# Performance work log

Hardware: AMD Instinct MI355X
Metric: run time of the kernel (lower is better)

Reference implementation:

```python
import jax, jax.numpy as jnp
import numpy as np

B, P, ENC = 64, 49, 1280
T, V, E, H, A = 25, 10000, 512, 1024, 512


def setup_inputs() -> dict:
    key = jax.random.key(0)
    ks = jax.random.split(key, 20)
    s = 0.02
    return {
        "encoder_out": jax.random.normal(ks[0], (B, P, ENC), jnp.float32),
        "captions": jax.random.randint(ks[1], (B, T), 0, V, jnp.int32),
        "embed": jax.random.normal(ks[2], (V, E), jnp.float32) * s,
        "W_eatt": jax.random.normal(ks[3], (A, ENC), jnp.float32) * s,
        "b_eatt": jnp.zeros((A,), jnp.float32),
        "W_datt": jax.random.normal(ks[4], (A, H), jnp.float32) * s,
        "b_datt": jnp.zeros((A,), jnp.float32),
        "W_fatt": jax.random.normal(ks[5], (1, A), jnp.float32) * s,
        "b_fatt": jnp.zeros((1,), jnp.float32),
        "W_ih": jax.random.normal(ks[6], (4 * H, E + ENC), jnp.float32) * s,
        "b_ih": jnp.zeros((4 * H,), jnp.float32),
        "W_hh": jax.random.normal(ks[7], (4 * H, H), jnp.float32) * s,
        "b_hh": jnp.zeros((4 * H,), jnp.float32),
        "W_h0": jax.random.normal(ks[8], (H, ENC), jnp.float32) * s,
        "b_h0": jnp.zeros((H,), jnp.float32),
        "W_c0": jax.random.normal(ks[9], (H, ENC), jnp.float32) * s,
        "b_c0": jnp.zeros((H,), jnp.float32),
        "W_out": jax.random.normal(ks[10], (V, H), jnp.float32) * s,
        "b_out": jnp.zeros((V,), jnp.float32),
    }


def reference(encoder_out, captions, embed, W_eatt, b_eatt, W_datt, b_datt,
              W_fatt, b_fatt, W_ih, b_ih, W_hh, b_hh, W_h0, b_h0, W_c0, b_c0,
              W_out, b_out):
    emb = embed[captions]                       # [B,T,E]
    mean_enc = encoder_out.mean(axis=1)         # [B,ENC]
    h0 = mean_enc @ W_h0.T + b_h0               # [B,H]
    c0 = mean_enc @ W_c0.T + b_c0
    # encoder-side attention projection is step-invariant; hoist out of loop
    att1 = encoder_out @ W_eatt.T + b_eatt      # [B,P,A]
    nH = h0.shape[-1]

    def step(carry, x_t):
        h, c = carry
        att2 = h @ W_datt.T + b_datt                          # [B,A]
        e = (jax.nn.relu(att1 + att2[:, None, :]) @ W_fatt.T + b_fatt)[..., 0]  # [B,P]
        alpha = jax.nn.softmax(e, axis=1)
        ctx = jnp.einsum('bp,bpe->be', alpha, encoder_out)    # [B,ENC]
        gin = jnp.concatenate([x_t, ctx], axis=1)             # [B,E+ENC]
        gates = gin @ W_ih.T + b_ih + h @ W_hh.T + b_hh       # [B,4H]
        i, f, g, o = jnp.split(gates, 4, axis=1)
        c_new = jax.nn.sigmoid(f) * c + jax.nn.sigmoid(i) * jnp.tanh(g)
        h_new = jax.nn.sigmoid(o) * jnp.tanh(c_new)
        preds = h_new @ W_out.T + b_out                       # dropout in eval mode = identity
        return (h_new, c_new), preds

    xs = jnp.swapaxes(emb[:, :-1, :], 0, 1)     # [T-1,B,E]
    _, preds = jax.lax.scan(step, (h0, c0), xs)
    return jnp.swapaxes(preds, 0, 1)            # [B,T-1,V]
```

## Files before the change

### kernel.cpp

```cpp
#include <hip/hip_runtime.h>
#include <hip/hip_bf16.h>

typedef float  v4f __attribute__((ext_vector_type(4)));
typedef short  v8s __attribute__((ext_vector_type(8)));
typedef int    v4i __attribute__((ext_vector_type(4)));

#define DEV static __device__ __forceinline__

DEV float bf2f(unsigned short u) {
    union { unsigned int i; float f; } x; x.i = ((unsigned int)u) << 16; return x.f;
}
DEV unsigned short f2bf(float f) {
    union { float f; unsigned int i; } x; x.f = f;
    unsigned int r = x.i + 0x7fff + ((x.i >> 16) & 1);
    return (unsigned short)(r >> 16);
}
DEV float sigm(float x) { return 1.f / (1.f + __expf(-x)); }

DEV v4i pack8(const float* f) {
    v4i o;
#pragma unroll
    for (int q = 0; q < 4; ++q)
        ((unsigned int*)&o)[q] = (unsigned int)f2bf(f[2 * q]) |
                                 ((unsigned int)f2bf(f[2 * q + 1]) << 16);
    return o;
}
DEV float lo16(unsigned int x) { union { unsigned int i; float f; } u; u.i = x << 16; return u.f; }
DEV float hi16(unsigned int x) { union { unsigned int i; float f; } u; u.i = x & 0xffff0000u; return u.f; }

__global__ __launch_bounds__(256) void uber_init(
    const float* __restrict__ Wih, const float* __restrict__ Whh,
    const float* __restrict__ bih, const float* __restrict__ bhh,
    const float* __restrict__ WoutF, const float* __restrict__ WeattF,
    const float* __restrict__ WdattF, const float* __restrict__ Wh0F,
    const float* __restrict__ Wc0F, const float* __restrict__ enc,
    const int* __restrict__ caps, const float* __restrict__ embed,
    unsigned short* __restrict__ Wz, unsigned short* __restrict__ Woutb,
    unsigned short* __restrict__ Weattb, unsigned short* __restrict__ Wdattb,
    unsigned short* __restrict__ Wh0b, unsigned short* __restrict__ Wc0b,
    unsigned short* __restrict__ encb, unsigned short* __restrict__ embb,
    unsigned short* __restrict__ meanb, float* __restrict__ bz)
{
    const int i = (blockIdx.x * 256 + threadIdx.x) * 8;
    float f[8];
    if (i < 11534336) {
        int n = i / 2816, k = i - n * 2816;
        const float* src = (k < 1792) ? &Wih[n * 1792 + k] : &Whh[n * 1024 + (k - 1792)];
        *(v4f*)&f[0] = *(const v4f*)src; *(v4f*)&f[4] = *(const v4f*)(src + 4);
        *(v4i*)&Wz[i] = pack8(f);
    } else if (i < 21774336) {
        int j = i - 11534336;
        *(v4f*)&f[0] = *(const v4f*)&WoutF[j]; *(v4f*)&f[4] = *(const v4f*)&WoutF[j + 4];
        *(v4i*)&Woutb[j] = pack8(f);
    } else if (i < 22429696) {
        int j = i - 21774336;
        *(v4f*)&f[0] = *(const v4f*)&WeattF[j]; *(v4f*)&f[4] = *(const v4f*)&WeattF[j + 4];
        *(v4i*)&Weattb[j] = pack8(f);
    } else if (i < 22953984) {
        int j = i - 22429696;
        *(v4f*)&f[0] = *(const v4f*)&WdattF[j]; *(v4f*)&f[4] = *(const v4f*)&WdattF[j + 4];
        *(v4i*)&Wdattb[j] = pack8(f);
    } else if (i < 24264704) {
        int j = i - 22953984;
        *(v4f*)&f[0] = *(const v4f*)&Wh0F[j]; *(v4f*)&f[4] = *(const v4f*)&Wh0F[j + 4];
        *(v4i*)&Wh0b[j] = pack8(f);
    } else if (i < 25575424) {
        int j = i - 24264704;
        *(v4f*)&f[0] = *(const v4f*)&Wc0F[j]; *(v4f*)&f[4] = *(const v4f*)&Wc0F[j + 4];
        *(v4i*)&Wc0b[j] = pack8(f);
    } else if (i < 29589504) {
        int j = i - 25575424;
        *(v4f*)&f[0] = *(const v4f*)&enc[j]; *(v4f*)&f[4] = *(const v4f*)&enc[j + 4];
        *(v4i*)&encb[j] = pack8(f);
    } else if (i < 30375936) {
        int j = i - 29589504;
        int b = j / 12288, r = j - b * 12288, t = r / 512, e = r - t * 512;
        const float* src = &embed[caps[b * 25 + t] * 512 + e];
        *(v4f*)&f[0] = *(const v4f*)src; *(v4f*)&f[4] = *(const v4f*)(src + 4);
        *(v4i*)&embb[j] = pack8(f);
    } else if (i < 30457856) {
        int j = i - 30375936;
        int b = j / 1280, c = j - b * 1280;
#pragma unroll
        for (int q = 0; q < 8; ++q) f[q] = 0.f;
        for (int p = 0; p < 49; ++p) {
            const float* src = &enc[(b * 49 + p) * 1280 + c];
            v4f a = *(const v4f*)src, bq = *(const v4f*)(src + 4);
#pragma unroll
            for (int q = 0; q < 4; ++q) { f[q] += a[q]; f[q + 4] += bq[q]; }
        }
#pragma unroll
        for (int q = 0; q < 8; ++q) f[q] *= (1.f / 49.f);
        *(v4i*)&meanb[j] = pack8(f);
    } else if (i < 30461952) {
        int j = i - 30457856;
#pragma unroll
        for (int q = 0; q < 8; ++q) f[q] = bih[j + q] + bhh[j + q];
        *(v4f*)&bz[j] = *(v4f*)&f[0]; *(v4f*)&bz[j + 4] = *(v4f*)&f[4];
    }
}

template <int OUT_BF16>
__global__ __launch_bounds__(256) void gemm64_bn16(
    const unsigned short* __restrict__ Ag, int lda,
    const unsigned short* __restrict__ Bg, int K,
    const float* __restrict__ bias, void* __restrict__ Cg, int ldc)
{
    __shared__ unsigned short lA[64 * 264];
    __shared__ unsigned short lB[16 * 264];
    const int tid = threadIdx.x, lane = tid & 63, w = tid >> 6;
    const int nb = blockIdx.x * 16;
    const int rA = tid >> 5, cA = (tid & 31) * 8;
    v4f acc = {0.f, 0.f, 0.f, 0.f};
    v4i ra[8], rb[2];
#pragma unroll
    for (int i = 0; i < 8; ++i)
        ra[i] = *(const v4i*)&Ag[(rA + i * 8) * lda + cA];
#pragma unroll
    for (int i = 0; i < 2; ++i)
        rb[i] = *(const v4i*)&Bg[(nb + rA + i * 8) * K + cA];
    for (int kt = 0; kt < K; kt += 256) {
#pragma unroll
        for (int i = 0; i < 8; ++i) *(v4i*)&lA[(rA + i * 8) * 264 + cA] = ra[i];
#pragma unroll
        for (int i = 0; i < 2; ++i) *(v4i*)&lB[(rA + i * 8) * 264 + cA] = rb[i];
        __syncthreads();
        if (kt + 256 < K) {
#pragma unroll
            for (int i = 0; i < 8; ++i)
                ra[i] = *(const v4i*)&Ag[(rA + i * 8) * lda + kt + 256 + cA];
#pragma unroll
            for (int i = 0; i < 2; ++i)
                rb[i] = *(const v4i*)&Bg[(nb + rA + i * 8) * K + kt + 256 + cA];
        }
#pragma unroll
        for (int ks = 0; ks < 8; ++ks) {
            v8s a = *(const v8s*)&lA[(w * 16 + (lane & 15)) * 264 + ks * 32 + (lane >> 4) * 8];
            v8s b = *(const v8s*)&lB[(lane & 15) * 264 + ks * 32 + (lane >> 4) * 8];
            acc = __builtin_amdgcn_mfma_f32_16x16x32_bf16(a, b, acc, 0, 0, 0);
        }
        __syncthreads();
    }
    const int n = nb + (lane & 15);
    const float bs = bias[n];
#pragma unroll
    for (int r = 0; r < 4; ++r) {
        int m = w * 16 + (lane >> 4) * 4 + r;
        float v = acc[r] + bs;
        if (OUT_BF16) ((unsigned short*)Cg)[m * ldc + n] = f2bf(v);
        else          ((float*)Cg)[m * ldc + n] = v;
    }
}

__global__ __launch_bounds__(256) void gemm_att1_k(
    const unsigned short* __restrict__ Aenc, const unsigned short* __restrict__ Bw,
    const float* __restrict__ bias, unsigned short* __restrict__ Cout)
{
    __shared__ unsigned short lA[64 * 136];
    __shared__ unsigned short lB[64 * 136];
    const int tid = threadIdx.x, lane = tid & 63, w = tid >> 6;
    const int mb = blockIdx.y * 64, nb = blockIdx.x * 64;
    const int rT = tid >> 4, cT = (tid & 15) * 8;
    v4f acc[4];
#pragma unroll
    for (int f = 0; f < 4; ++f) acc[f] = (v4f){0.f, 0.f, 0.f, 0.f};
    v4i ra[4], rb[4];
#pragma unroll
    for (int i = 0; i < 4; ++i) {
        ra[i] = *(const v4i*)&Aenc[(mb + rT + i * 16) * 1280 + cT];
        rb[i] = *(const v4i*)&Bw[(nb + rT + i * 16) * 1280 + cT];
    }
    for (int kt = 0; kt < 1280; kt += 128) {
#pragma unroll
        for (int i = 0; i < 4; ++i) {
            *(v4i*)&lA[(rT + i * 16) * 136 + cT] = ra[i];
            *(v4i*)&lB[(rT + i * 16) * 136 + cT] = rb[i];
        }
        __syncthreads();
        if (kt + 128 < 1280) {
#pragma unroll
            for (int i = 0; i < 4; ++i) {
                ra[i] = *(const v4i*)&Aenc[(mb + rT + i * 16) * 1280 + kt + 128 + cT];
                rb[i] = *(const v4i*)&Bw[(nb + rT + i * 16) * 1280 + kt + 128 + cT];
            }
        }
#pragma unroll
        for (int ks = 0; ks < 4; ++ks) {
            v8s a = *(const v8s*)&lA[(w * 16 + (lane & 15)) * 136 + ks * 32 + (lane >> 4) * 8];
#pragma unroll
            for (int f = 0; f < 4; ++f) {
                v8s b = *(const v8s*)&lB[(f * 16 + (lane & 15)) * 136 + ks * 32 + (lane >> 4) * 8];
                acc[f] = __builtin_amdgcn_mfma_f32_16x16x32_bf16(a, b, acc[f], 0, 0, 0);
            }
        }
        __syncthreads();
    }
#pragma unroll
    for (int f = 0; f < 4; ++f) {
        int n = nb + f * 16 + (lane & 15);
        float bs = bias[n];
#pragma unroll
        for (int r = 0; r < 4; ++r) {
            int m = mb + w * 16 + (lane >> 4) * 4 + r;
            Cout[m * 512 + n] = f2bf(acc[f][r] + bs);
        }
    }
}

__global__ __launch_bounds__(256) void attn_ctx_k(
    const float* __restrict__ att2, const unsigned short* __restrict__ att1b,
    const float* __restrict__ Wfatt, const float* __restrict__ bfatt,
    const unsigned short* __restrict__ encb, const unsigned short* __restrict__ embb,
    unsigned short* __restrict__ z, int tstep)
{
    __shared__ float a2[512];
    __shared__ float wf[512];
    __shared__ float es[64];
    __shared__ float alpha[64];
    const int tid = threadIdx.x, lane = tid & 63, w = tid >> 6;
    const int b = blockIdx.x;
    a2[tid]       = att2[b * 512 + tid];
    a2[tid + 256] = att2[b * 512 + tid + 256];
    wf[tid]       = Wfatt[tid];
    wf[tid + 256] = Wfatt[tid + 256];
    __syncthreads();
    for (int p = w; p < 49; p += 4) {
        v4i u = *(const v4i*)&att1b[(b * 49 + p) * 512 + lane * 8];
        v4f c0 = *(const v4f*)&a2[lane * 8], c1 = *(const v4f*)&a2[lane * 8 + 4];
        v4f w0 = *(const v4f*)&wf[lane * 8], w1 = *(const v4f*)&wf[lane * 8 + 4];
        float s = 0.f;
#pragma unroll
        for (int q = 0; q < 4; ++q) {
            unsigned int x = ((unsigned int*)&u)[q];
            float vlo = lo16(x), vhi = hi16(x);
            float clo = (q < 2) ? c0[q * 2] : c1[q * 2 - 4];
            float chi = (q < 2) ? c0[q * 2 + 1] : c1[q * 2 - 3];
            float wlo = (q < 2) ? w0[q * 2] : w1[q * 2 - 4];
            float whi = (q < 2) ? w0[q * 2 + 1] : w1[q * 2 - 3];
            s += fmaxf(vlo + clo, 0.f) * wlo;
            s += fmaxf(vhi + chi, 0.f) * whi;
        }
#pragma unroll
        for (int off = 32; off > 0; off >>= 1) s += __shfl_xor(s, off);
        if (lane == 0) es[p] = s + bfatt[0];
    }
    __syncthreads();
    if (w == 0) {
        float v = (lane < 49) ? es[lane] : -1e30f;
        float m = v;
#pragma unroll
        for (int off = 32; off > 0; off >>= 1) m = fmaxf(m, __shfl_xor(m, off));
        float e = (lane < 49) ? __expf(v - m) : 0.f;
        float s = e;
#pragma unroll
        for (int off = 32; off > 0; off >>= 1) s += __shfl_xor(s, off);
        if (lane < 49) alpha[lane] = e / s;
    }
    __syncthreads();
    if (tid < 160) {
        const int jb = tid * 8;
        float acc[8];
#pragma unroll
        for (int q = 0; q < 8; ++q) acc[q] = 0.f;
        for (int p = 0; p < 49; ++p) {
            v4i u = *(const v4i*)&encb[(b * 49 + p) * 1280 + jb];
            float al = alpha[p];
#pragma unroll
            for (int q = 0; q < 4; ++q) {
                unsigned int x = ((unsigned int*)&u)[q];
                acc[2 * q]     += al * lo16(x);
                acc[2 * q + 1] += al * hi16(x);
            }
        }
        *(v4i*)&z[b * 2816 + 512 + jb] = pack8(acc);
    }
    if (tid < 64)
        *(v4i*)&z[b * 2816 + tid * 8] = *(const v4i*)&embb[(b * 24 + tstep) * 512 + tid * 8];
}

__global__ __launch_bounds__(256) void gates_lstm_k(
    const unsigned short* __restrict__ z, const unsigned short* __restrict__ Wz,
    const float* __restrict__ bz, float* __restrict__ cst,
    unsigned short* __restrict__ zh, unsigned short* __restrict__ HallT)
{
    __shared__ unsigned short lA[64 * 264];
    __shared__ unsigned short lB[16 * 264];
    __shared__ float gbuf[64 * 20];
    const int tid = threadIdx.x, lane = tid & 63, w = tid >> 6;
    const int hb = blockIdx.x * 4;
    const int rT = tid >> 5, cT = (tid & 31) * 8;
    const int gate = rT & 3, hco = rT >> 2;
    const int growB = (gate * 1024 + hb + hco) * 2816;
    const int growB2 = (((rT + 8) & 3) * 1024 + hb + ((rT + 8) >> 2)) * 2816;
    v4f acc = {0.f, 0.f, 0.f, 0.f};
    v4i ra[8], rb[2];
#pragma unroll
    for (int i = 0; i < 8; ++i)
        ra[i] = *(const v4i*)&z[(rT + i * 8) * 2816 + cT];
    rb[0] = *(const v4i*)&Wz[growB + cT];
    rb[1] = *(const v4i*)&Wz[growB2 + cT];
    for (int kt = 0; kt < 2816; kt += 256) {
#pragma unroll
        for (int i = 0; i < 8; ++i) *(v4i*)&lA[(rT + i * 8) * 264 + cT] = ra[i];
        *(v4i*)&lB[rT * 264 + cT] = rb[0];
        *(v4i*)&lB[(rT + 8) * 264 + cT] = rb[1];
        __syncthreads();
        if (kt + 256 < 2816) {
#pragma unroll
            for (int i = 0; i < 8; ++i)
                ra[i] = *(const v4i*)&z[(rT + i * 8) * 2816 + kt + 256 + cT];
            rb[0] = *(const v4i*)&Wz[growB + kt + 256 + cT];
            rb[1] = *(const v4i*)&Wz[growB2 + kt + 256 + cT];
        }
#pragma unroll
        for (int ks = 0; ks < 8; ++ks) {
            v8s a = *(const v8s*)&lA[(w * 16 + (lane & 15)) * 264 + ks * 32 + (lane >> 4) * 8];
            v8s b = *(const v8s*)&lB[(lane & 15) * 264 + ks * 32 + (lane >> 4) * 8];
            acc = __builtin_amdgcn_mfma_f32_16x16x32_bf16(a, b, acc, 0, 0, 0);
        }
        __syncthreads();
    }
#pragma unroll
    for (int r = 0; r < 4; ++r) {
        int m = w * 16 + (lane >> 4) * 4 + r;
        int n = lane & 15;
        gbuf[m * 20 + n] = acc[r];
    }
    __syncthreads();
    const int b = tid >> 2, hc2 = tid & 3, hidx = hb + hc2;
    float gi = gbuf[b * 20 + hc2 * 4 + 0] + bz[hidx];
    float gf = gbuf[b * 20 + hc2 * 4 + 1] + bz[1024 + hidx];
    float gg = gbuf[b * 20 + hc2 * 4 + 2] + bz[2048 + hidx];
    float go = gbuf[b * 20 + hc2 * 4 + 3] + bz[3072 + hidx];
    float cn = sigm(gf) * cst[b * 1024 + hidx] + sigm(gi) * tanhf(gg);
    float hn = sigm(go) * tanhf(cn);
    cst[b * 1024 + hidx] = cn;
    unsigned short hb16 = f2bf(hn);
    zh[b * 2816 + hidx] = hb16;
    HallT[b * 1024 + hidx] = hb16;
}

__global__ __launch_bounds__(256) void preds_k(
    const unsigned short* __restrict__ Hall, const unsigned short* __restrict__ Wout,
    const float* __restrict__ bout, float* __restrict__ out)
{
    __shared__ unsigned short lA[128 * 72];
    __shared__ unsigned short lB[128 * 72];
    const int tid = threadIdx.x, lane = tid & 63, w = tid >> 6;
    const int mb = blockIdx.y * 128, nb = blockIdx.x * 128;
    const int rT = tid >> 3, cT = (tid & 7) * 8;
    int nB = nb + rT; if (nB > 9999) nB = 9999;
    v4f acc[2][8];
#pragma unroll
    for (int i = 0; i < 2; ++i)
#pragma unroll
        for (int f = 0; f < 8; ++f) acc[i][f] = (v4f){0.f, 0.f, 0.f, 0.f};
    v4i ra[4], rb[4];
#pragma unroll
    for (int i = 0; i < 4; ++i) {
        ra[i] = *(const v4i*)&Hall[(mb + rT + i * 32) * 1024 + cT];
        int n2 = nb + rT + i * 32; if (n2 > 9999) n2 = 9999;
        rb[i] = *(const v4i*)&Wout[n2 * 1024 + cT];
    }
    for (int kt = 0; kt < 1024; kt += 64) {
#pragma unroll
        for (int i = 0; i < 4; ++i) {
            *(v4i*)&lA[(rT + i * 32) * 72 + cT] = ra[i];
            *(v4i*)&lB[(rT + i * 32) * 72 + cT] = rb[i];
        }
        __syncthreads();
        if (kt + 64 < 1024) {
#pragma unroll
            for (int i = 0; i < 4; ++i) {
                ra[i] = *(const v4i*)&Hall[(mb + rT + i * 32) * 1024 + kt + 64 + cT];
                int n2 = nb + rT + i * 32; if (n2 > 9999) n2 = 9999;
                rb[i] = *(const v4i*)&Wout[n2 * 1024 + kt + 64 + cT];
            }
        }
#pragma unroll
        for (int ks = 0; ks < 2; ++ks) {
            int ko = ks * 32 + (lane >> 4) * 8;
            v8s a0 = *(const v8s*)&lA[(w * 32 + (lane & 15)) * 72 + ko];
            v8s a1 = *(const v8s*)&lA[(w * 32 + 16 + (lane & 15)) * 72 + ko];
#pragma unroll
            for (int f = 0; f < 8; ++f) {
                v8s b = *(const v8s*)&lB[(f * 16 + (lane & 15)) * 72 + ko];
                acc[0][f] = __builtin_amdgcn_mfma_f32_16x16x32_bf16(a0, b, acc[0][f], 0, 0, 0);
                acc[1][f] = __builtin_amdgcn_mfma_f32_16x16x32_bf16(a1, b, acc[1][f], 0, 0, 0);
            }
        }
        __syncthreads();
    }
#pragma unroll
    for (int f = 0; f < 8; ++f) {
        int n = nb + f * 16 + (lane & 15);
        if (n < 10000) {
            float bs = bout[n];
#pragma unroll
            for (int i = 0; i < 2; ++i)
#pragma unroll
                for (int r = 0; r < 4; ++r) {
                    int m = mb + w * 32 + i * 16 + (lane >> 4) * 4 + r;
                    int tt = m >> 6, bb = m & 63;
                    out[(bb * 24 + tt) * 10000 + n] = acc[i][f][r] + bs;
                }
        }
    }
}

extern "C" void kernel_launch(void* const* d_in, const int* in_sizes, int n_in,
                              void* d_out, int out_size, void* d_ws, size_t ws_size,
                              hipStream_t stream)
{
    const float* enc   = (const float*)d_in[0];
    const int*   caps  = (const int*)d_in[1];
    const float* embed = (const float*)d_in[2];
    const float* Weatt = (const float*)d_in[3];
    const float* beatt = (const float*)d_in[4];
    const float* Wdatt = (const float*)d_in[5];
    const float* bdatt = (const float*)d_in[6];
    const float* Wfatt = (const float*)d_in[7];
    const float* bfatt = (const float*)d_in[8];
    const float* Wih   = (const float*)d_in[9];
    const float* bih   = (const float*)d_in[10];
    const float* Whh   = (const float*)d_in[11];
    const float* bhh   = (const float*)d_in[12];
    const float* Wh0   = (const float*)d_in[13];
    const float* bh0   = (const float*)d_in[14];
    const float* Wc0   = (const float*)d_in[15];
    const float* bc0   = (const float*)d_in[16];
    const float* WoutF = (const float*)d_in[17];
    const float* bout  = (const float*)d_in[18];
    float* out = (float*)d_out;

    char* ws = (char*)d_ws;
    size_t off = 0;
    auto carve = [&](size_t bytes) -> void* {
        void* p = ws + off; off += (bytes + 255) & ~(size_t)255; return p;
    };
    unsigned short* Wzb    = (unsigned short*)carve(11534336ull * 2);
    unsigned short* Woutb  = (unsigned short*)carve(10240000ull * 2);
    unsigned short* Weattb = (unsigned short*)carve(655360ull * 2);
    unsigned short* Wdattb = (unsigned short*)carve(524288ull * 2);
    unsigned short* Wh0b   = (unsigned short*)carve(1310720ull * 2);
    unsigned short* Wc0b   = (unsigned short*)carve(1310720ull * 2);
    unsigned short* encb   = (unsigned short*)carve(4014080ull * 2);
    unsigned short* embb   = (unsigned short*)carve(786432ull * 2);
    unsigned short* meanb  = (unsigned short*)carve(81920ull * 2);
    unsigned short* att1b  = (unsigned short*)carve(1605632ull * 2);
    unsigned short* Hallb  = (unsigned short*)carve(1572864ull * 2);
    unsigned short* zb     = (unsigned short*)carve(180224ull * 2);
    float* bz   = (float*)carve(4096ull * 4);
    float* att2 = (float*)carve(32768ull * 4);
    float* cst  = (float*)carve(65536ull * 4);

    uber_init<<<14874, 256, 0, stream>>>(Wih, Whh, bih, bhh, WoutF, Weatt, Wdatt,
        Wh0, Wc0, enc, caps, embed, Wzb, Woutb, Weattb, Wdattb, Wh0b, Wc0b,
        encb, embb, meanb, bz);

    gemm64_bn16<1><<<64, 256, 0, stream>>>(meanb, 1280, Wh0b, 1280, bh0, zb + 1792, 2816);
    gemm64_bn16<0><<<64, 256, 0, stream>>>(meanb, 1280, Wc0b, 1280, bc0, cst, 1024);

    gemm_att1_k<<<dim3(8, 49), 256, 0, stream>>>(encb, Weattb, beatt, att1b);

    for (int t = 0; t < 24; ++t) {
        gemm64_bn16<0><<<32, 256, 0, stream>>>(zb + 1792, 2816, Wdattb, 1024, bdatt, att2, 512);
        attn_ctx_k<<<64, 256, 0, stream>>>(att2, att1b, Wfatt, bfatt, encb, embb, zb, t);
        gates_lstm_k<<<256, 256, 0, stream>>>(zb, Wzb, bz, cst, zb + 1792,
                                              Hallb + (size_t)t * 64 * 1024);
    }

    preds_k<<<dim3(79, 12), 256, 0, stream>>>(Hallb, Woutb, bout, out);
}
```

Baseline: 1.137 ms.

## Replace per-step LSTM kernel launches with a persistent grid-barrier kernel

```diff
diff --git a/kernel.cpp b/kernel.cpp
--- a/kernel.cpp
+++ b/kernel.cpp
@@ -28,58 +28,62 @@
 DEV float lo16(unsigned int x) { union { unsigned int i; float f; } u; u.i = x << 16; return u.f; }
 DEV float hi16(unsigned int x) { union { unsigned int i; float f; } u; u.i = x & 0xffff0000u; return u.f; }
 
+__global__ void bar_init_k(int* __restrict__ bars) {
+    bars[blockIdx.x * 256 + threadIdx.x] = 0;
+}
+
+DEV void gridbar(int* bars, int idx) {
+    __syncthreads();
+    if (threadIdx.x == 0) {
+        __builtin_amdgcn_fence(__ATOMIC_RELEASE, "");
+        int* base = bars + idx * 160;
+        const int grp = blockIdx.x & 7;
+        int old = __hip_atomic_fetch_add(base + grp * 16, 1, __ATOMIC_RELAXED,
+                                         __HIP_MEMORY_SCOPE_SYSTEM);
+        if (old == 31) {
+            int og = __hip_atomic_fetch_add(base + 128, 1, __ATOMIC_RELAXED,
+                                            __HIP_MEMORY_SCOPE_SYSTEM);
+            if (og == 7)
+                __hip_atomic_store(base + 144, 1, __ATOMIC_RELAXED,
+                                   __HIP_MEMORY_SCOPE_SYSTEM);
+        }
+        while (!__hip_atomic_load(base + 144, __ATOMIC_RELAXED,
+                                  __HIP_MEMORY_SCOPE_SYSTEM))
+            __builtin_amdgcn_s_sleep(2);
+        __builtin_amdgcn_fence(__ATOMIC_ACQUIRE, "");
+    }
+    __syncthreads();
+}
+
 __global__ __launch_bounds__(256) void uber_init(
-    const float* __restrict__ Wih, const float* __restrict__ Whh,
-    const float* __restrict__ bih, const float* __restrict__ bhh,
     const float* __restrict__ WoutF, const float* __restrict__ WeattF,
-    const float* __restrict__ WdattF, const float* __restrict__ Wh0F,
-    const float* __restrict__ Wc0F, const float* __restrict__ enc,
-    const int* __restrict__ caps, const float* __restrict__ embed,
-    unsigned short* __restrict__ Wz, unsigned short* __restrict__ Woutb,
-    unsigned short* __restrict__ Weattb, unsigned short* __restrict__ Wdattb,
-    unsigned short* __restrict__ Wh0b, unsigned short* __restrict__ Wc0b,
+    const float* __restrict__ enc, const int* __restrict__ caps,
+    const float* __restrict__ embed,
+    unsigned short* __restrict__ Woutb, unsigned short* __restrict__ Weattb,
     unsigned short* __restrict__ encb, unsigned short* __restrict__ embb,
-    unsigned short* __restrict__ meanb, float* __restrict__ bz)
+    float* __restrict__ meanf)
 {
     const int i = (blockIdx.x * 256 + threadIdx.x) * 8;
     float f[8];
-    if (i < 11534336) {
-        int n = i / 2816, k = i - n * 2816;
-        const float* src = (k < 1792) ? &Wih[n * 1792 + k] : &Whh[n * 1024 + (k - 1792)];
-        *(v4f*)&f[0] = *(const v4f*)src; *(v4f*)&f[4] = *(const v4f*)(src + 4);
-        *(v4i*)&Wz[i] = pack8(f);
-    } else if (i < 21774336) {
-        int j = i - 11534336;
-        *(v4f*)&f[0] = *(const v4f*)&WoutF[j]; *(v4f*)&f[4] = *(const v4f*)&WoutF[j + 4];
-        *(v4i*)&Woutb[j] = pack8(f);
-    } else if (i < 22429696) {
-        int j = i - 21774336;
+    if (i < 10240000) {
+        *(v4f*)&f[0] = *(const v4f*)&WoutF[i]; *(v4f*)&f[4] = *(const v4f*)&WoutF[i + 4];
+        *(v4i*)&Woutb[i] = pack8(f);
+    } else if (i < 10895360) {
+        int j = i - 10240000;
         *(v4f*)&f[0] = *(const v4f*)&WeattF[j]; *(v4f*)&f[4] = *(const v4f*)&WeattF[j + 4];
         *(v4i*)&Weattb[j] = pack8(f);
-    } else if (i < 22953984) {
-        int j = i - 22429696;
-        *(v4f*)&f[0] = *(const v4f*)&WdattF[j]; *(v4f*)&f[4] = *(const v4f*)&WdattF[j + 4];
-        *(v4i*)&Wdattb[j] = pack8(f);
-    } else if (i < 24264704) {
-        int j = i - 22953984;
-        *(v4f*)&f[0] = *(const v4f*)&Wh0F[j]; *(v4f*)&f[4] = *(const v4f*)&Wh0F[j + 4];
-        *(v4i*)&Wh0b[j] = pack8(f);
-    } else if (i < 25575424) {
-        int j = i - 24264704;
-        *(v4f*)&f[0] = *(const v4f*)&Wc0F[j]; *(v4f*)&f[4] = *(const v4f*)&Wc0F[j + 4];
-        *(v4i*)&Wc0b[j] = pack8(f);
-    } else if (i < 29589504) {
-        int j = i - 25575424;
+    } else if (i < 14909440) {
+        int j = i - 10895360;
         *(v4f*)&f[0] = *(const v4f*)&enc[j]; *(v4f*)&f[4] = *(const v4f*)&enc[j + 4];
         *(v4i*)&encb[j] = pack8(f);
-    } else if (i < 30375936) {
-        int j = i - 29589504;
+    } else if (i < 15695872) {
+        int j = i - 14909440;
         int b = j / 12288, r = j - b * 12288, t = r / 512, e = r - t * 512;
         const float* src = &embed[caps[b * 25 + t] * 512 + e];
         *(v4f*)&f[0] = *(const v4f*)src; *(v4f*)&f[4] = *(const v4f*)(src + 4);
         *(v4i*)&embb[j] = pack8(f);
-    } else if (i < 30457856) {
-        int j = i - 30375936;
+    } else if (i < 15777792) {
+        int j = i - 15695872;
         int b = j / 1280, c = j - b * 1280;
 #pragma unroll
         for (int q = 0; q < 8; ++q) f[q] = 0.f;
@@ -91,64 +95,8 @@
         }
 #pragma unroll
         for (int q = 0; q < 8; ++q) f[q] *= (1.f / 49.f);
-        *(v4i*)&meanb[j] = pack8(f);
-    } else if (i < 30461952) {
-        int j = i - 30457856;
-#pragma unroll
-        for (int q = 0; q < 8; ++q) f[q] = bih[j + q] + bhh[j + q];
-        *(v4f*)&bz[j] = *(v4f*)&f[0]; *(v4f*)&bz[j + 4] = *(v4f*)&f[4];
-    }
-}
-
-template <int OUT_BF16>
-__global__ __launch_bounds__(256) void gemm64_bn16(
-    const unsigned short* __restrict__ Ag, int lda,
-    const unsigned short* __restrict__ Bg, int K,
-    const float* __restrict__ bias, void* __restrict__ Cg, int ldc)
-{
-    __shared__ unsigned short lA[64 * 264];
-    __shared__ unsigned short lB[16 * 264];
-    const int tid = threadIdx.x, lane = tid & 63, w = tid >> 6;
-    const int nb = blockIdx.x * 16;
-    const int rA = tid >> 5, cA = (tid & 31) * 8;
-    v4f acc = {0.f, 0.f, 0.f, 0.f};
-    v4i ra[8], rb[2];
-#pragma unroll
-    for (int i = 0; i < 8; ++i)
-        ra[i] = *(const v4i*)&Ag[(rA + i * 8) * lda + cA];
-#pragma unroll
-    for (int i = 0; i < 2; ++i)
-        rb[i] = *(const v4i*)&Bg[(nb + rA + i * 8) * K + cA];
-    for (int kt = 0; kt < K; kt += 256) {
-#pragma unroll
-        for (int i = 0; i < 8; ++i) *(v4i*)&lA[(rA + i * 8) * 264 + cA] = ra[i];
-#pragma unroll
-        for (int i = 0; i < 2; ++i) *(v4i*)&lB[(rA + i * 8) * 264 + cA] = rb[i];
-        __syncthreads();
-        if (kt + 256 < K) {
-#pragma unroll
-            for (int i = 0; i < 8; ++i)
-                ra[i] = *(const v4i*)&Ag[(rA + i * 8) * lda + kt + 256 + cA];
-#pragma unroll
-            for (int i = 0; i < 2; ++i)
-                rb[i] = *(const v4i*)&Bg[(nb + rA + i * 8) * K + kt + 256 + cA];
-        }
-#pragma unroll
-        for (int ks = 0; ks < 8; ++ks) {
-            v8s a = *(const v8s*)&lA[(w * 16 + (lane & 15)) * 264 + ks * 32 + (lane >> 4) * 8];
-            v8s b = *(const v8s*)&lB[(lane & 15) * 264 + ks * 32 + (lane >> 4) * 8];
-            acc = __builtin_amdgcn_mfma_f32_16x16x32_bf16(a, b, acc, 0, 0, 0);
-        }
-        __syncthreads();
-    }
-    const int n = nb + (lane & 15);
-    const float bs = bias[n];
-#pragma unroll
-    for (int r = 0; r < 4; ++r) {
-        int m = w * 16 + (lane >> 4) * 4 + r;
-        float v = acc[r] + bs;
-        if (OUT_BF16) ((unsigned short*)Cg)[m * ldc + n] = f2bf(v);
-        else          ((float*)Cg)[m * ldc + n] = v;
+        *(v4f*)&meanf[j] = *(v4f*)&f[0];
+        *(v4f*)&meanf[j + 4] = *(v4f*)&f[4];
     }
 }
 
@@ -207,149 +155,211 @@
     }
 }
 
-__global__ __launch_bounds__(256) void attn_ctx_k(
-    const float* __restrict__ att2, const unsigned short* __restrict__ att1b,
+__global__ __launch_bounds__(256, 1) void pers_k(
+    const float* __restrict__ Wih, const float* __restrict__ Whh,
+    const float* __restrict__ bih, const float* __restrict__ bhh,
+    const float* __restrict__ Wdatt, const float* __restrict__ bdatt,
     const float* __restrict__ Wfatt, const float* __restrict__ bfatt,
-    const unsigned short* __restrict__ encb, const unsigned short* __restrict__ embb,
-    unsigned short* __restrict__ z, int tstep)
+    const float* __restrict__ Wh0, const float* __restrict__ bh0,
+    const float* __restrict__ Wc0, const float* __restrict__ bc0,
+    const float* __restrict__ meanf,
+    const unsigned short* __restrict__ att1b,
+    const unsigned short* __restrict__ encb,
+    const unsigned short* __restrict__ embb,
+    unsigned short* __restrict__ z, float* __restrict__ att2,
+    unsigned short* __restrict__ Hall, int* __restrict__ bars)
 {
-    __shared__ float a2[512];
+    __shared__ unsigned short lWz[16 * 2824];
+    __shared__ unsigned short lWd[16 * 1032];
+    __shared__ float gbuf[64 * 20];
+    __shared__ float a2f[512];
     __shared__ float wf[512];
     __shared__ float es[64];
     __shared__ float alpha[64];
+    __shared__ float bzs[16];
+
     const int tid = threadIdx.x, lane = tid & 63, w = tid >> 6;
-    const int b = blockIdx.x;
-    a2[tid]       = att2[b * 512 + tid];
-    a2[tid + 256] = att2[b * 512 + tid + 256];
-    wf[tid]       = Wfatt[tid];
-    wf[tid + 256] = Wfatt[tid + 256];
-    __syncthreads();
-    for (int p = w; p < 49; p += 4) {
-        v4i u = *(const v4i*)&att1b[(b * 49 + p) * 512 + lane * 8];
-        v4f c0 = *(const v4f*)&a2[lane * 8], c1 = *(const v4f*)&a2[lane * 8 + 4];
-        v4f w0 = *(const v4f*)&wf[lane * 8], w1 = *(const v4f*)&wf[lane * 8 + 4];
-        float s = 0.f;
-#pragma unroll
-        for (int q = 0; q < 4; ++q) {
-            unsigned int x = ((unsigned int*)&u)[q];
-            float vlo = lo16(x), vhi = hi16(x);
-            float clo = (q < 2) ? c0[q * 2] : c1[q * 2 - 4];
-            float chi = (q < 2) ? c0[q * 2 + 1] : c1[q * 2 - 3];
-            float wlo = (q < 2) ? w0[q * 2] : w1[q * 2 - 4];
-            float whi = (q < 2) ? w0[q * 2 + 1] : w1[q * 2 - 3];
-            s += fmaxf(vlo + clo, 0.f) * wlo;
-            s += fmaxf(vhi + chi, 0.f) * whi;
-        }
-#pragma unroll
-        for (int off = 32; off > 0; off >>= 1) s += __shfl_xor(s, off);
-        if (lane == 0) es[p] = s + bfatt[0];
-    }
-    __syncthreads();
-    if (w == 0) {
-        float v = (lane < 49) ? es[lane] : -1e30f;
-        float m = v;
-#pragma unroll
-        for (int off = 32; off > 0; off >>= 1) m = fmaxf(m, __shfl_xor(m, off));
-        float e = (lane < 49) ? __expf(v - m) : 0.f;
-        float s = e;
-#pragma unroll
-        for (int off = 32; off > 0; off >>= 1) s += __shfl_xor(s, off);
-        if (lane < 49) alpha[lane] = e / s;
-    }
-    __syncthreads();
-    if (tid < 160) {
-        const int jb = tid * 8;
-        float acc[8];
-#pragma unroll
-        for (int q = 0; q < 8; ++q) acc[q] = 0.f;
-        for (int p = 0; p < 49; ++p) {
-            v4i u = *(const v4i*)&encb[(b * 49 + p) * 1280 + jb];
-            float al = alpha[p];
-#pragma unroll
-            for (int q = 0; q < 4; ++q) {
-                unsigned int x = ((unsigned int*)&u)[q];
-                acc[2 * q]     += al * lo16(x);
-                acc[2 * q + 1] += al * hi16(x);
-            }
-        }
-        *(v4i*)&z[b * 2816 + 512 + jb] = pack8(acc);
-    }
-    if (tid < 64)
-        *(v4i*)&z[b * 2816 + tid * 8] = *(const v4i*)&embb[(b * 24 + tstep) * 512 + tid * 8];
-}
-
-__global__ __launch_bounds__(256) void gates_lstm_k(
-    const unsigned short* __restrict__ z, const unsigned short* __restrict__ Wz,
-    const float* __restrict__ bz, float* __restrict__ cst,
-    unsigned short* __restrict__ zh, unsigned short* __restrict__ HallT)
-{
-    __shared__ unsigned short lA[64 * 264];
-    __shared__ unsigned short lB[16 * 264];
-    __shared__ float gbuf[64 * 20];
-    const int tid = threadIdx.x, lane = tid & 63, w = tid >> 6;
-    const int hb = blockIdx.x * 4;
-    const int rT = tid >> 5, cT = (tid & 31) * 8;
-    const int gate = rT & 3, hco = rT >> 2;
-    const int growB = (gate * 1024 + hb + hco) * 2816;
-    const int growB2 = (((rT + 8) & 3) * 1024 + hb + ((rT + 8) >> 2)) * 2816;
-    v4f acc = {0.f, 0.f, 0.f, 0.f};
-    v4i ra[8], rb[2];
-#pragma unroll
-    for (int i = 0; i < 8; ++i)
-        ra[i] = *(const v4i*)&z[(rT + i * 8) * 2816 + cT];
-    rb[0] = *(const v4i*)&Wz[growB + cT];
-    rb[1] = *(const v4i*)&Wz[growB2 + cT];
-    for (int kt = 0; kt < 2816; kt += 256) {
-#pragma unroll
-        for (int i = 0; i < 8; ++i) *(v4i*)&lA[(rT + i * 8) * 264 + cT] = ra[i];
-        *(v4i*)&lB[rT * 264 + cT] = rb[0];
-        *(v4i*)&lB[(rT + 8) * 264 + cT] = rb[1];
-        __syncthreads();
-        if (kt + 256 < 2816) {
-#pragma unroll
-            for (int i = 0; i < 8; ++i)
-                ra[i] = *(const v4i*)&z[(rT + i * 8) * 2816 + kt + 256 + cT];
-            rb[0] = *(const v4i*)&Wz[growB + kt + 256 + cT];
-            rb[1] = *(const v4i*)&Wz[growB2 + kt + 256 + cT];
-        }
-#pragma unroll
-        for (int ks = 0; ks < 8; ++ks) {
-            v8s a = *(const v8s*)&lA[(w * 16 + (lane & 15)) * 264 + ks * 32 + (lane >> 4) * 8];
-            v8s b = *(const v8s*)&lB[(lane & 15) * 264 + ks * 32 + (lane >> 4) * 8];
-            acc = __builtin_amdgcn_mfma_f32_16x16x32_bf16(a, b, acc, 0, 0, 0);
-        }
-        __syncthreads();
-    }
-#pragma unroll
-    for (int r = 0; r < 4; ++r) {
-        int m = w * 16 + (lane >> 4) * 4 + r;
-        int n = lane & 15;
-        gbuf[m * 20 + n] = acc[r];
-    }
-    __syncthreads();
-    const int b = tid >> 2, hc2 = tid & 3, hidx = hb + hc2;
-    float gi = gbuf[b * 20 + hc2 * 4 + 0] + bz[hidx];
-    float gf = gbuf[b * 20 + hc2 * 4 + 1] + bz[1024 + hidx];
-    float gg = gbuf[b * 20 + hc2 * 4 + 2] + bz[2048 + hidx];
-    float go = gbuf[b * 20 + hc2 * 4 + 3] + bz[3072 + hidx];
-    float cn = sigm(gf) * cst[b * 1024 + hidx] + sigm(gi) * tanhf(gg);
-    float hn = sigm(go) * tanhf(cn);
-    cst[b * 1024 + hidx] = cn;
-    unsigned short hb16 = f2bf(hn);
-    zh[b * 2816 + hidx] = hb16;
-    HallT[b * 1024 + hidx] = hb16;
+    const int g = blockIdx.x;
+
+    for (int r = 0; r < 16; ++r) {
+        const int grow = (r & 3) * 1024 + g * 4 + (r >> 2);
+        for (int c = tid * 8; c < 2816; c += 2048) {
+            float f[8];
+            const float* src = (c < 1792) ? &Wih[grow * 1792 + c]
+                                          : &Whh[grow * 1024 + (c - 1792)];
+            *(v4f*)&f[0] = *(const v4f*)src;
+            *(v4f*)&f[4] = *(const v4f*)(src + 4);
+            *(v4i*)&lWz[r * 2824 + c] = pack8(f);
+        }
+    }
+    if (g < 32) {
+        for (int r = 0; r < 16; ++r) {
+            const int arow = g * 16 + r;
+            for (int c = tid * 8; c < 1024; c += 2048) {
+                float f[8];
+                *(v4f*)&f[0] = *(const v4f*)&Wdatt[arow * 1024 + c];
+                *(v4f*)&f[4] = *(const v4f*)&Wdatt[arow * 1024 + c + 4];
+                *(v4i*)&lWd[r * 1032 + c] = pack8(f);
+            }
+        }
+    }
+    if (tid < 16) {
+        const int grow = (tid & 3) * 1024 + g * 4 + (tid >> 2);
+        bzs[tid] = bih[grow] + bhh[grow];
+    }
+    wf[tid] = Wfatt[tid]; wf[tid + 256] = Wfatt[tid + 256];
+    const float bf0 = bfatt[0];
+
+    const int bb0 = tid >> 2, hc0 = tid & 3, hidx0 = g * 4 + hc0;
+    float sh = bh0[hidx0], creg = bc0[hidx0];
+    for (int k = 0; k < 1280; k += 4) {
+        v4f mv = *(const v4f*)&meanf[bb0 * 1280 + k];
+        v4f wh = *(const v4f*)&Wh0[hidx0 * 1280 + k];
+        v4f wc = *(const v4f*)&Wc0[hidx0 * 1280 + k];
+#pragma unroll
+        for (int q = 0; q < 4; ++q) { sh += mv[q] * wh[q]; creg += mv[q] * wc[q]; }
+    }
+    z[bb0 * 2816 + 1792 + hidx0] = f2bf(sh);
+
+    int barid = 0;
+    gridbar(bars, barid++);
+
+    for (int t = 0; t < 24; ++t) {
+        unsigned short* zcur = z + (t & 1) * 180224;
+        unsigned short* znxt = z + ((t + 1) & 1) * 180224;
+
+        if (g < 32) {
+            const unsigned short* zh = zcur + 1792;
+            const int mrow = w * 16 + (lane & 15);
+            const int ko = (lane >> 4) * 8;
+            v4f acc0 = {0.f,0.f,0.f,0.f}, acc1 = {0.f,0.f,0.f,0.f};
+#pragma unroll 4
+            for (int kt = 0; kt < 32; kt += 2) {
+                v8s a0 = *(const v8s*)&zh[mrow * 2816 + kt * 32 + ko];
+                v8s b0 = *(const v8s*)&lWd[(lane & 15) * 1032 + kt * 32 + ko];
+                acc0 = __builtin_amdgcn_mfma_f32_16x16x32_bf16(a0, b0, acc0, 0, 0, 0);
+                v8s a1 = *(const v8s*)&zh[mrow * 2816 + kt * 32 + 32 + ko];
+                v8s b1 = *(const v8s*)&lWd[(lane & 15) * 1032 + kt * 32 + 32 + ko];
+                acc1 = __builtin_amdgcn_mfma_f32_16x16x32_bf16(a1, b1, acc1, 0, 0, 0);
+            }
+            const int n = g * 16 + (lane & 15);
+#pragma unroll
+            for (int r = 0; r < 4; ++r)
+                att2[(w * 16 + (lane >> 4) * 4 + r) * 512 + n] = acc0[r] + acc1[r];
+        }
+        gridbar(bars, barid++);
+
+        {
+            const int b = g & 63, q = g >> 6;
+            a2f[tid]       = att2[b * 512 + tid] + bdatt[tid];
+            a2f[tid + 256] = att2[b * 512 + tid + 256] + bdatt[tid + 256];
+            __syncthreads();
+            for (int p = w; p < 49; p += 4) {
+                v4i u = *(const v4i*)&att1b[(b * 49 + p) * 512 + lane * 8];
+                float s = 0.f;
+#pragma unroll
+                for (int qq = 0; qq < 4; ++qq) {
+                    unsigned int x = ((unsigned int*)&u)[qq];
+                    int a0 = lane * 8 + 2 * qq, a1 = a0 + 1;
+                    s += fmaxf(lo16(x) + a2f[a0], 0.f) * wf[a0];
+                    s += fmaxf(hi16(x) + a2f[a1], 0.f) * wf[a1];
+                }
+#pragma unroll
+                for (int off = 32; off > 0; off >>= 1) s += __shfl_xor(s, off);
+                if (lane == 0) es[p] = s + bf0;
+            }
+            __syncthreads();
+            if (w == 0) {
+                float v = (lane < 49) ? es[lane] : -1e30f;
+                float m = v;
+#pragma unroll
+                for (int off = 32; off > 0; off >>= 1) m = fmaxf(m, __shfl_xor(m, off));
+                float e = (lane < 49) ? __expf(v - m) : 0.f;
+                float s = e;
+#pragma unroll
+                for (int off = 32; off > 0; off >>= 1) s += __shfl_xor(s, off);
+                if (lane < 49) alpha[lane] = e / s;
+            }
+            __syncthreads();
+            if (tid < 40) {
+                const int jb = q * 320 + tid * 8;
+                float acc8[8];
+#pragma unroll
+                for (int qq = 0; qq < 8; ++qq) acc8[qq] = 0.f;
+#pragma unroll 7
+                for (int p = 0; p < 49; ++p) {
+                    v4i u = *(const v4i*)&encb[(b * 49 + p) * 1280 + jb];
+                    float al = alpha[p];
+#pragma unroll
+                    for (int qq = 0; qq < 4; ++qq) {
+                        unsigned int x = ((unsigned int*)&u)[qq];
+                        acc8[2 * qq]     += al * lo16(x);
+                        acc8[2 * qq + 1] += al * hi16(x);
+                    }
+                }
+                *(v4i*)&zcur[b * 2816 + 512 + jb] = pack8(acc8);
+            }
+        }
+        gridbar(bars, barid++);
+
+        {
+            const int mrow = w * 16 + (lane & 15);
+            const int ko = (lane >> 4) * 8;
+            v4f acc0 = {0.f,0.f,0.f,0.f}, acc1 = {0.f,0.f,0.f,0.f};
+#pragma unroll 4
+            for (int kt = 0; kt < 16; kt += 2) {
+                v8s a0 = *(const v8s*)&embb[(mrow * 24 + t) * 512 + kt * 32 + ko];
+                v8s b0 = *(const v8s*)&lWz[(lane & 15) * 2824 + kt * 32 + ko];
+                acc0 = __builtin_amdgcn_mfma_f32_16x16x32_bf16(a0, b0, acc0, 0, 0, 0);
+                v8s a1 = *(const v8s*)&embb[(mrow * 24 + t) * 512 + kt * 32 + 32 + ko];
+                v8s b1 = *(const v8s*)&lWz[(lane & 15) * 2824 + kt * 32 + 32 + ko];
+                acc1 = __builtin_amdgcn_mfma_f32_16x16x32_bf16(a1, b1, acc1, 0, 0, 0);
+            }
+#pragma unroll 4
+            for (int kt = 16; kt < 88; kt += 2) {
+                v8s a0 = *(const v8s*)&zcur[mrow * 2816 + kt * 32 + ko];
+                v8s b0 = *(const v8s*)&lWz[(lane & 15) * 2824 + kt * 32 + ko];
+                acc0 = __builtin_amdgcn_mfma_f32_16x16x32_bf16(a0, b0, acc0, 0, 0, 0);
+                v8s a1 = *(const v8s*)&zcur[mrow * 2816 + kt * 32 + 32 + ko];
+                v8s b1 = *(const v8s*)&lWz[(lane & 15) * 2824 + kt * 32 + 32 + ko];
+                acc1 = __builtin_amdgcn_mfma_f32_16x16x32_bf16(a1, b1, acc1, 0, 0, 0);
+            }
+#pragma unroll
+            for (int r = 0; r < 4; ++r)
+                gbuf[(w * 16 + (lane >> 4) * 4 + r) * 20 + (lane & 15)] =
+                    acc0[r] + acc1[r];
+            __syncthreads();
+            const int b = tid >> 2, hc2 = tid & 3, hidx = g * 4 + hc2;
+            float gi = gbuf[b * 20 + hc2 * 4 + 0] + bzs[hc2 * 4 + 0];
+            float gf = gbuf[b * 20 + hc2 * 4 + 1] + bzs[hc2 * 4 + 1];
+            float gg = gbuf[b * 20 + hc2 * 4 + 2] + bzs[hc2 * 4 + 2];
+            float go = gbuf[b * 20 + hc2 * 4 + 3] + bzs[hc2 * 4 + 3];
+            float cn = sigm(gf) * creg + sigm(gi) * tanhf(gg);
+            float hn = sigm(go) * tanhf(cn);
+            creg = cn;
+            unsigned short hb16 = f2bf(hn);
+            znxt[b * 2816 + 1792 + hidx] = hb16;
+            Hall[t * 65536 + b * 1024 + hidx] = hb16;
+        }
+        if (t != 23) gridbar(bars, barid++);
+    }
 }
 
 __global__ __launch_bounds__(256) void preds_k(
     const unsigned short* __restrict__ Hall, const unsigned short* __restrict__ Wout,
     const float* __restrict__ bout, float* __restrict__ out)
 {
+    const int bid = blockIdx.x;
+    const int x = bid & 7, q = bid >> 3;
+    int m, n;
+    if (x < 7) { m = q / 10; n = x * 10 + q % 10; }
+    else       { m = q / 9;  n = 70 + q % 9; if (m >= 12) return; }
+    const int mb = m * 128, nb = n * 128;
+
     __shared__ unsigned short lA[128 * 72];
     __shared__ unsigned short lB[128 * 72];
     const int tid = threadIdx.x, lane = tid & 63, w = tid >> 6;
-    const int mb = blockIdx.y * 128, nb = blockIdx.x * 128;
     const int rT = tid >> 3, cT = (tid & 7) * 8;
-    int nB = nb + rT; if (nB > 9999) nB = 9999;
     v4f acc[2][8];
 #pragma unroll
     for (int i = 0; i < 2; ++i)
@@ -393,16 +403,16 @@
     }
 #pragma unroll
     for (int f = 0; f < 8; ++f) {
-        int n = nb + f * 16 + (lane & 15);
-        if (n < 10000) {
-            float bs = bout[n];
+        int nn = nb + f * 16 + (lane & 15);
+        if (nn < 10000) {
+            float bs = bout[nn];
 #pragma unroll
             for (int i = 0; i < 2; ++i)
 #pragma unroll
                 for (int r = 0; r < 4; ++r) {
-                    int m = mb + w * 32 + i * 16 + (lane >> 4) * 4 + r;
-                    int tt = m >> 6, bb = m & 63;
-                    out[(bb * 24 + tt) * 10000 + n] = acc[i][f][r] + bs;
+                    int mm = mb + w * 32 + i * 16 + (lane >> 4) * 4 + r;
+                    int tt = mm >> 6, bb = mm & 63;
+                    out[(bb * 24 + tt) * 10000 + nn] = acc[i][f][r] + bs;
                 }
         }
     }
@@ -438,37 +448,26 @@
     auto carve = [&](size_t bytes) -> void* {
         void* p = ws + off; off += (bytes + 255) & ~(size_t)255; return p;
     };
-    unsigned short* Wzb    = (unsigned short*)carve(11534336ull * 2);
     unsigned short* Woutb  = (unsigned short*)carve(10240000ull * 2);
     unsigned short* Weattb = (unsigned short*)carve(655360ull * 2);
-    unsigned short* Wdattb = (unsigned short*)carve(524288ull * 2);
-    unsigned short* Wh0b   = (unsigned short*)carve(1310720ull * 2);
-    unsigned short* Wc0b   = (unsigned short*)carve(1310720ull * 2);
     unsigned short* encb   = (unsigned short*)carve(4014080ull * 2);
     unsigned short* embb   = (unsigned short*)carve(786432ull * 2);
-    unsigned short* meanb  = (unsigned short*)carve(81920ull * 2);
+    float*          meanf  = (float*)carve(81920ull * 4);
     unsigned short* att1b  = (unsigned short*)carve(1605632ull * 2);
     unsigned short* Hallb  = (unsigned short*)carve(1572864ull * 2);
-    unsigned short* zb     = (unsigned short*)carve(180224ull * 2);
-    float* bz   = (float*)carve(4096ull * 4);
+    unsigned short* zb     = (unsigned short*)carve(360448ull * 2);
     float* att2 = (float*)carve(32768ull * 4);
-    float* cst  = (float*)carve(65536ull * 4);
-
-    uber_init<<<14874, 256, 0, stream>>>(Wih, Whh, bih, bhh, WoutF, Weatt, Wdatt,
-        Wh0, Wc0, enc, caps, embed, Wzb, Woutb, Weattb, Wdattb, Wh0b, Wc0b,
-        encb, embb, meanb, bz);
-
-    gemm64_bn16<1><<<64, 256, 0, stream>>>(meanb, 1280, Wh0b, 1280, bh0, zb + 1792, 2816);
-    gemm64_bn16<0><<<64, 256, 0, stream>>>(meanb, 1280, Wc0b, 1280, bc0, cst, 1024);
+    int*   bars = (int*)carve(11520ull * 4);
+
+    bar_init_k<<<45, 256, 0, stream>>>(bars);
+
+    uber_init<<<7704, 256, 0, stream>>>(WoutF, Weatt, enc, caps, embed,
+        Woutb, Weattb, encb, embb, meanf);
 
     gemm_att1_k<<<dim3(8, 49), 256, 0, stream>>>(encb, Weattb, beatt, att1b);
 
-    for (int t = 0; t < 24; ++t) {
-        gemm64_bn16<0><<<32, 256, 0, stream>>>(zb + 1792, 2816, Wdattb, 1024, bdatt, att2, 512);
-        attn_ctx_k<<<64, 256, 0, stream>>>(att2, att1b, Wfatt, bfatt, encb, embb, zb, t);
-        gates_lstm_k<<<256, 256, 0, stream>>>(zb, Wzb, bz, cst, zb + 1792,
-                                              Hallb + (size_t)t * 64 * 1024);
-    }
-
-    preds_k<<<dim3(79, 12), 256, 0, stream>>>(Hallb, Woutb, bout, out);
-}
+    pers_k<<<256, 256, 0, stream>>>(Wih, Whh, bih, bhh, Wdatt, bdatt, Wfatt, bfatt,
+        Wh0, bh0, Wc0, bc0, meanf, att1b, encb, embb, zb, att2, Hallb, bars);
+
+    preds_k<<<960, 256, 0, stream>>>(Hallb, Woutb, bout, out);
+}
```

Measured after the change: 1.512 ms. +33.0%, slower.
